# Optimization experiments

Measured on AMD Instinct MI355X. Metric: run time of the kernel, lower is better.

The kernel has to match this reference:

```python
import jax, jax.numpy as jnp
import numpy as np
from jax import lax

# NARX hyperparameters (match init_kwargs)
D_I, D_O, D_X, D_Y, D_HL = 8, 8, 32, 16, 256
B, T = 2048, 512
IN_SIZE = D_I * D_X + D_O * D_Y  # 384


def setup_inputs() -> dict:
    key = jax.random.key(0)
    k1, k2, k3, k4, k5 = jax.random.split(key, 5)
    s1 = 1.0 / np.sqrt(IN_SIZE).astype(np.float32)
    s2 = 1.0 / np.sqrt(D_HL).astype(np.float32)
    x = jax.random.normal(k1, (B, T, D_X), dtype=jnp.float32)
    W1 = jax.random.uniform(k2, (D_HL, IN_SIZE), jnp.float32, -s1, s1)
    b1 = jax.random.uniform(k3, (D_HL,), jnp.float32, -s1, s1)
    W2 = jax.random.uniform(k4, (D_Y, D_HL), jnp.float32, -s2, s2)
    b2 = jax.random.uniform(k5, (D_Y,), jnp.float32, -s2, s2)
    return {"x": x, "W1": W1, "b1": b1, "W2": W2, "b2": b2}


def reference(x, W1, b1, W2, b2):
    # Closed-loop NARX: mode='close', y=None, bootstrap=None.
    # y_pred starts as zeros; loop runs from max(d_i, d_o) to T.
    Bb, Tt, _ = x.shape
    start = max(D_I, D_O)

    def step(hist, t):
        # hist: [B, d_o, d_y], oldest first == y_pred[:, t-d_o:t, :]
        xw = lax.dynamic_slice_in_dim(x, t - D_I, D_I, axis=1).reshape(Bb, D_I * D_X)
        inp = jnp.concatenate([xw, hist.reshape(Bb, D_O * D_Y)], axis=1)
        h = jnp.tanh(inp @ W1.T + b1)
        out = jax.nn.sigmoid(h @ W2.T + b2)  # act2 = Sigmoid
        new_hist = jnp.concatenate([hist[:, 1:, :], out[:, None, :]], axis=1)
        return new_hist, out

    hist0 = jnp.zeros((Bb, D_O, D_Y), dtype=x.dtype)  # zero-initialized y_pred history
    _, outs = lax.scan(step, hist0, jnp.arange(start, Tt))
    outs = jnp.transpose(outs, (1, 0, 2))  # [B, T-start, d_y]
    prefix = jnp.zeros((Bb, start, D_Y), dtype=x.dtype)
    return jnp.concatenate([prefix, outs], axis=1)  # [B, T, d_y]
```

## Files before the change

### kernel.cpp

```cpp
#include <hip/hip_runtime.h>
#include <hip/hip_bf16.h>


typedef short bf16x8 __attribute__((ext_vector_type(8)));
typedef float f32x4  __attribute__((ext_vector_type(4)));

#define MFMA16(A,B,C) __builtin_amdgcn_mfma_f32_16x16x32_bf16((A),(B),(C),0,0,0)

constexpr int DT = 512;
constexpr int DX = 32;
constexpr int DY = 16;
constexpr int BB = 16;

constexpr int YROW  = 24;
constexpr int YSLOT = 16 * YROW;
constexpr int HROW  = 40;
constexpr int HWAVE = 16 * HROW;
constexpr int PROW  = 18;
constexpr int PWAVE = 16 * PROW;

__device__ __forceinline__ short bfbits(float f) {
  return __builtin_bit_cast(short, (__bf16)f);
}
__device__ __forceinline__ float fast_tanh(float a) {
  float e = __expf(2.0f * a);
  return 1.0f - 2.0f * __builtin_amdgcn_rcpf(e + 1.0f);
}
__device__ __forceinline__ float fast_sigmoid(float a) {
  return __builtin_amdgcn_rcpf(1.0f + __expf(-a));
}

__global__ __launch_bounds__(512, 2) void narx_kernel(
    const float* __restrict__ x,  const float* __restrict__ W1,
    const float* __restrict__ b1, const float* __restrict__ W2,
    const float* __restrict__ b2, float* __restrict__ out)
{
  __shared__ __align__(16) short ybuf[8 * YSLOT];
  __shared__ __align__(16) short hbuf[8 * HWAVE];
  __shared__ __align__(16) float pbuf[8 * PWAVE];

  const int tid  = threadIdx.x;
  const int lane = tid & 63;
  const int w    = tid >> 6;
  const int lm   = lane & 15;
  const int lg   = lane >> 4;
  const int b0   = blockIdx.x * BB;

  bf16x8 wf[2][12];
#pragma unroll
  for (int ti = 0; ti < 2; ++ti) {
    const int n = w * 32 + ti * 16 + lm;
#pragma unroll
    for (int c = 0; c < 12; ++c) {
      const float* p = W1 + n * 384 + c * 32 + lg * 8;
      bf16x8 v;
#pragma unroll
      for (int j = 0; j < 8; ++j) v[j] = bfbits(p[j]);
      wf[ti][c] = v;
    }
  }
  bf16x8 w2fp;
  {
    const float* p = W2 + lm * 256 + w * 32 + lg * 8;
    bf16x8 v;
#pragma unroll
    for (int j = 0; j < 8; ++j) v[j] = bfbits(p[j]);
    w2fp = v;
  }
  const float b1v0 = b1[w * 32 + lm];
  const float b1v1 = b1[w * 32 + 16 + lm];
  const float b2v  = b2[lm];

  {
    const int m = tid >> 5, off = (tid & 31) * 4;
    f32x4 z = {0.f, 0.f, 0.f, 0.f};
    *reinterpret_cast<f32x4*>(out + (size_t)(b0 + m) * (DT * DY) + off) = z;
  }

  const float* xlane = x + (size_t)(b0 + lm) * (DT * DX) + lg * 8;
  bf16x8 xr[8];
#pragma unroll
  for (int s = 0; s < 8; ++s) {
    f32x4 a = *reinterpret_cast<const f32x4*>(xlane + s * DX);
    f32x4 b = *reinterpret_cast<const f32x4*>(xlane + s * DX + 4);
    bf16x8 v;
#pragma unroll
    for (int j = 0; j < 4; ++j) { v[j] = bfbits(a[j]); v[4 + j] = bfbits(b[j]); }
    xr[s] = v;
  }
  f32x4 gA0 = *reinterpret_cast<const f32x4*>(xlane + 8 * DX);
  f32x4 gA1 = *reinterpret_cast<const f32x4*>(xlane + 8 * DX + 4);
  f32x4 gB0 = gA0, gB1 = gA1;

  for (int i = tid; i < 8 * YSLOT; i += 512) ybuf[i] = 0;
  __syncthreads();

  const int yhalf  = lg >> 1;
  const int yoff   = lm * YROW + (lg & 1) * 8;
  const int hw_w   = w * HWAVE;
  const int hswz_w = lg << 3;
  const int hread  = hw_w + ((lm * HROW + lg * 8) ^ (((lm >> 2) & 3) << 3));
  const int pw     = w * PWAVE;
  const int rrow   = tid >> 4, rcol = tid & 15;

#define STEP(U, CUR0, CUR1, NXT0, NXT1)                                        \
  do {                                                                         \
    const int t = tb + (U);                                                    \
    { const int tl = (t + 1 < DT) ? (t + 1) : (DT - 1);                        \
      NXT0 = *reinterpret_cast<const f32x4*>(xlane + tl * DX);                 \
      NXT1 = *reinterpret_cast<const f32x4*>(xlane + tl * DX + 4); }           \
    bf16x8 ay0, ay1, ay2, ay3;                                                 \
    ay0 = *reinterpret_cast<const bf16x8*>(                                    \
        &ybuf[((((U) + 0 + yhalf) & 7) * YSLOT) + yoff]);                      \
    ay1 = *reinterpret_cast<const bf16x8*>(                                    \
        &ybuf[((((U) + 2 + yhalf) & 7) * YSLOT) + yoff]);                      \
    ay2 = *reinterpret_cast<const bf16x8*>(                                    \
        &ybuf[((((U) + 4 + yhalf) & 7) * YSLOT) + yoff]);                      \
    ay3 = *reinterpret_cast<const bf16x8*>(                                    \
        &ybuf[((((U) + 6 + yhalf) & 7) * YSLOT) + yoff]);                      \
    f32x4 acc0a = {0.f,0.f,0.f,0.f}, acc0b = {0.f,0.f,0.f,0.f};                \
    f32x4 acc1a = {0.f,0.f,0.f,0.f}, acc1b = {0.f,0.f,0.f,0.f};                \
    _Pragma("unroll") for (int c = 0; c < 6; ++c) {                            \
      acc0a = MFMA16(xr[((U) + c) & 7], wf[0][c], acc0a);                      \
      acc1a = MFMA16(xr[((U) + c) & 7], wf[1][c], acc1a);                      \
    }                                                                          \
    acc0b = MFMA16(xr[((U) + 6) & 7], wf[0][6], acc0b);                        \
    acc1b = MFMA16(xr[((U) + 6) & 7], wf[1][6], acc1b);                        \
    acc0b = MFMA16(xr[((U) + 7) & 7], wf[0][7], acc0b);                        \
    acc1b = MFMA16(xr[((U) + 7) & 7], wf[1][7], acc1b);                        \
    acc0b = MFMA16(ay0, wf[0][8],  acc0b);  acc1b = MFMA16(ay0, wf[1][8],  acc1b); \
    acc0b = MFMA16(ay1, wf[0][9],  acc0b);  acc1b = MFMA16(ay1, wf[1][9],  acc1b); \
    acc0b = MFMA16(ay2, wf[0][10], acc0b);  acc1b = MFMA16(ay2, wf[1][10], acc1b); \
    acc0b = MFMA16(ay3, wf[0][11], acc0b);  acc1b = MFMA16(ay3, wf[1][11], acc1b); \
    { bf16x8 nx;                                                               \
      _Pragma("unroll") for (int j = 0; j < 4; ++j) {                          \
        nx[j] = bfbits(CUR0[j]); nx[4 + j] = bfbits(CUR1[j]); }                \
      xr[(U) & 7] = nx; }                                                      \
    _Pragma("unroll") for (int r = 0; r < 4; ++r) {                            \
      const int row = lg * 4 + r;                                              \
      const float h0 = fast_tanh(acc0a[r] + acc0b[r] + b1v0);                  \
      const float h1 = fast_tanh(acc1a[r] + acc1b[r] + b1v1);                  \
      hbuf[hw_w + ((row * HROW + lm) ^ hswz_w)]      = bfbits(h0);             \
      hbuf[hw_w + ((row * HROW + 16 + lm) ^ hswz_w)] = bfbits(h1);             \
    }                                                                          \
    bf16x8 ha = *reinterpret_cast<const bf16x8*>(&hbuf[hread]);                \
    f32x4 pz = {0.f, 0.f, 0.f, 0.f};                                           \
    f32x4 part = MFMA16(ha, w2fp, pz);                                         \
    _Pragma("unroll") for (int r = 0; r < 4; ++r)                              \
      pbuf[pw + (lg * 4 + r) * PROW + lm] = part[r];                           \
    __syncthreads();                                                           \
    if (tid < 256) {                                                           \
      float s = b2v;                                                           \
      _Pragma("unroll") for (int ww = 0; ww < 8; ++ww)                         \
        s += pbuf[ww * PWAVE + rrow * PROW + rcol];                            \
      const float o = fast_sigmoid(s);                                         \
      ybuf[((U) & 7) * YSLOT + rrow * YROW + rcol] = bfbits(o);                \
      out[(size_t)(b0 + rrow) * (DT * DY) + t * DY + rcol] = o;                \
    }                                                                          \
    __syncthreads();                                                           \
  } while (0)

  for (int tb = 8; tb < DT; tb += 8) {
    STEP(0, gA0, gA1, gB0, gB1);
    STEP(1, gB0, gB1, gA0, gA1);
    STEP(2, gA0, gA1, gB0, gB1);
    STEP(3, gB0, gB1, gA0, gA1);
    STEP(4, gA0, gA1, gB0, gB1);
    STEP(5, gB0, gB1, gA0, gA1);
    STEP(6, gA0, gA1, gB0, gB1);
    STEP(7, gB0, gB1, gA0, gA1);
  }
#undef STEP
}

extern "C" void kernel_launch(void* const* d_in, const int* in_sizes, int n_in,
                              void* d_out, int out_size, void* d_ws, size_t ws_size,
                              hipStream_t stream) {
  const float* x  = (const float*)d_in[0];
  const float* W1 = (const float*)d_in[1];
  const float* b1 = (const float*)d_in[2];
  const float* W2 = (const float*)d_in[3];
  const float* b2 = (const float*)d_in[4];
  float* out = (float*)d_out;
  narx_kernel<<<dim3(128), dim3(512), 0, stream>>>(x, W1, b1, W2, b2, out);
}
```

Baseline: 649.9 us.

## Keep y-history in registers with shift-window and pack h pairs into 32-bit LDS

Each step now reads only the newest y slot from LDS and keeps the older history in a four-register sliding window. Lane groups shift this window on alternating steps, and a second set of W1 history fragments covers the odd-step lane layout. The hidden activations are written as packed bf16 pairs in 32-bit LDS words, and W2 columns are permuted to match, which halves the number of hidden-state LDS stores. This cuts per-step LDS traffic in the serial recurrence, at the cost of extra registers for the additional W1 fragments and the history window.

Measured after the change: 651.0 us. Within noise of the previous version (+0.2%).

```diff
diff --git a/kernel.cpp b/kernel.cpp
--- a/kernel.cpp
+++ b/kernel.cpp
@@ -14,8 +14,8 @@
 
 constexpr int YROW  = 24;
 constexpr int YSLOT = 16 * YROW;
-constexpr int HROW  = 40;
-constexpr int HWAVE = 16 * HROW;
+constexpr int H32ROW = 20;
+constexpr int H32WAVE = 16 * H32ROW;
 constexpr int PROW  = 18;
 constexpr int PWAVE = 16 * PROW;
 
@@ -36,7 +36,7 @@
     const float* __restrict__ b2, float* __restrict__ out)
 {
   __shared__ __align__(16) short ybuf[8 * YSLOT];
-  __shared__ __align__(16) short hbuf[8 * HWAVE];
+  __shared__ __align__(16) unsigned int hbuf32[8 * H32WAVE];
   __shared__ __align__(16) float pbuf[8 * PWAVE];
 
   const int tid  = threadIdx.x;
@@ -59,13 +59,25 @@
       wf[ti][c] = v;
     }
   }
+  bf16x8 wfo[2][4];
+#pragma unroll
+  for (int ti = 0; ti < 2; ++ti) {
+    const int n = w * 32 + ti * 16 + lm;
+#pragma unroll
+    for (int c = 0; c < 4; ++c) {
+      const float* p = W1 + n * 384 + 256 + c * 32 + (lg ^ 2) * 8;
+      bf16x8 v;
+#pragma unroll
+      for (int j = 0; j < 8; ++j) v[j] = bfbits(p[j]);
+      wfo[ti][c] = v;
+    }
+  }
   bf16x8 w2fp;
-  {
-    const float* p = W2 + lm * 256 + w * 32 + lg * 8;
-    bf16x8 v;
-#pragma unroll
-    for (int j = 0; j < 8; ++j) v[j] = bfbits(p[j]);
-    w2fp = v;
+#pragma unroll
+  for (int j = 0; j < 8; ++j) {
+    const int p = lg * 8 + j;
+    const int col = (p & 1) ? (16 + (p >> 1)) : (p >> 1);
+    w2fp[j] = bfbits(W2[lm * 256 + w * 32 + col]);
   }
   const float b1v0 = b1[w * 32 + lm];
   const float b1v1 = b1[w * 32 + 16 + lm];
@@ -92,14 +104,16 @@
   f32x4 gA1 = *reinterpret_cast<const f32x4*>(xlane + 8 * DX + 4);
   f32x4 gB0 = gA0, gB1 = gA1;
 
+  bf16x8 yr0 = {0,0,0,0,0,0,0,0}, yr1 = {0,0,0,0,0,0,0,0};
+  bf16x8 yr2 = {0,0,0,0,0,0,0,0}, yr3 = {0,0,0,0,0,0,0,0};
+
   for (int i = tid; i < 8 * YSLOT; i += 512) ybuf[i] = 0;
   __syncthreads();
 
-  const int yhalf  = lg >> 1;
-  const int yoff   = lm * YROW + (lg & 1) * 8;
-  const int hw_w   = w * HWAVE;
-  const int hswz_w = lg << 3;
-  const int hread  = hw_w + ((lm * HROW + lg * 8) ^ (((lm >> 2) & 3) << 3));
+  const int g      = lg >> 1;
+  const int yfoff  = lm * YROW + (lg & 1) * 8;
+  const int hw32   = w * H32WAVE;
+  const int hread  = hw32 + lm * H32ROW + lg * 4;
   const int pw     = w * PWAVE;
   const int rrow   = tid >> 4, rcol = tid & 15;
 
@@ -109,15 +123,15 @@
     { const int tl = (t + 1 < DT) ? (t + 1) : (DT - 1);                        \
       NXT0 = *reinterpret_cast<const f32x4*>(xlane + tl * DX);                 \
       NXT1 = *reinterpret_cast<const f32x4*>(xlane + tl * DX + 4); }           \
-    bf16x8 ay0, ay1, ay2, ay3;                                                 \
-    ay0 = *reinterpret_cast<const bf16x8*>(                                    \
-        &ybuf[((((U) + 0 + yhalf) & 7) * YSLOT) + yoff]);                      \
-    ay1 = *reinterpret_cast<const bf16x8*>(                                    \
-        &ybuf[((((U) + 2 + yhalf) & 7) * YSLOT) + yoff]);                      \
-    ay2 = *reinterpret_cast<const bf16x8*>(                                    \
-        &ybuf[((((U) + 4 + yhalf) & 7) * YSLOT) + yoff]);                      \
-    ay3 = *reinterpret_cast<const bf16x8*>(                                    \
-        &ybuf[((((U) + 6 + yhalf) & 7) * YSLOT) + yoff]);                      \
+         \
+    { bf16x8 fresh = *reinterpret_cast<const bf16x8*>(                         \
+          &ybuf[(((U) + 7) & 7) * YSLOT + yfoff]);                             \
+      const bool ds_ = (g == (((U) + 1) & 1));                                 \
+      yr0 = ds_ ? yr1 : yr0;                                                   \
+      yr1 = ds_ ? yr2 : yr1;                                                   \
+      yr2 = ds_ ? yr3 : yr2;                                                   \
+      yr3 = ds_ ? fresh : yr3; }                                               \
+                   \
     f32x4 acc0a = {0.f,0.f,0.f,0.f}, acc0b = {0.f,0.f,0.f,0.f};                \
     f32x4 acc1a = {0.f,0.f,0.f,0.f}, acc1b = {0.f,0.f,0.f,0.f};                \
     _Pragma("unroll") for (int c = 0; c < 6; ++c) {                            \
@@ -128,22 +142,33 @@
     acc1b = MFMA16(xr[((U) + 6) & 7], wf[1][6], acc1b);                        \
     acc0b = MFMA16(xr[((U) + 7) & 7], wf[0][7], acc0b);                        \
     acc1b = MFMA16(xr[((U) + 7) & 7], wf[1][7], acc1b);                        \
-    acc0b = MFMA16(ay0, wf[0][8],  acc0b);  acc1b = MFMA16(ay0, wf[1][8],  acc1b); \
-    acc0b = MFMA16(ay1, wf[0][9],  acc0b);  acc1b = MFMA16(ay1, wf[1][9],  acc1b); \
-    acc0b = MFMA16(ay2, wf[0][10], acc0b);  acc1b = MFMA16(ay2, wf[1][10], acc1b); \
-    acc0b = MFMA16(ay3, wf[0][11], acc0b);  acc1b = MFMA16(ay3, wf[1][11], acc1b); \
+    if ((U) & 1) {       \
+      acc0b = MFMA16(yr0, wfo[0][0], acc0b); acc1b = MFMA16(yr0, wfo[1][0], acc1b); \
+      acc0b = MFMA16(yr1, wfo[0][1], acc0b); acc1b = MFMA16(yr1, wfo[1][1], acc1b); \
+      acc0b = MFMA16(yr2, wfo[0][2], acc0b); acc1b = MFMA16(yr2, wfo[1][2], acc1b); \
+      acc0b = MFMA16(yr3, wfo[0][3], acc0b); acc1b = MFMA16(yr3, wfo[1][3], acc1b); \
+    } else {                 \
+      acc0b = MFMA16(yr0, wf[0][8],  acc0b); acc1b = MFMA16(yr0, wf[1][8],  acc1b); \
+      acc0b = MFMA16(yr1, wf[0][9],  acc0b); acc1b = MFMA16(yr1, wf[1][9],  acc1b); \
+      acc0b = MFMA16(yr2, wf[0][10], acc0b); acc1b = MFMA16(yr2, wf[1][10], acc1b); \
+      acc0b = MFMA16(yr3, wf[0][11], acc0b); acc1b = MFMA16(yr3, wf[1][11], acc1b); \
+    }                                                                          \
+                      \
     { bf16x8 nx;                                                               \
       _Pragma("unroll") for (int j = 0; j < 4; ++j) {                          \
         nx[j] = bfbits(CUR0[j]); nx[4 + j] = bfbits(CUR1[j]); }                \
       xr[(U) & 7] = nx; }                                                      \
+       \
     _Pragma("unroll") for (int r = 0; r < 4; ++r) {                            \
       const int row = lg * 4 + r;                                              \
       const float h0 = fast_tanh(acc0a[r] + acc0b[r] + b1v0);                  \
       const float h1 = fast_tanh(acc1a[r] + acc1b[r] + b1v1);                  \
-      hbuf[hw_w + ((row * HROW + lm) ^ hswz_w)]      = bfbits(h0);             \
-      hbuf[hw_w + ((row * HROW + 16 + lm) ^ hswz_w)] = bfbits(h1);             \
-    }                                                                          \
-    bf16x8 ha = *reinterpret_cast<const bf16x8*>(&hbuf[hread]);                \
+      const unsigned int hp = (unsigned int)(unsigned short)bfbits(h0)         \
+                            | ((unsigned int)(unsigned short)bfbits(h1) << 16);\
+      hbuf32[hw32 + row * H32ROW + lm] = hp;                                   \
+    }                                                                          \
+        \
+    bf16x8 ha = *reinterpret_cast<const bf16x8*>(&hbuf32[hread]);              \
     f32x4 pz = {0.f, 0.f, 0.f, 0.f};                                           \
     f32x4 part = MFMA16(ha, w2fp, pz);                                         \
     _Pragma("unroll") for (int r = 0; r < 4; ++r)                              \
```
